# Optimization experiments

Measured on AMD Instinct MI355X. Metric: run time of the kernel, lower is better.

Reference implementation:

```python
import jax, jax.numpy as jnp
import numpy as np

NUM_REL = 3


def _edge_norm(dst, et, n_nodes):
    # PyG RGCNConv default aggr='mean': mean over edges per (dst, relation).
    seg = dst * NUM_REL + et
    cnt = jax.ops.segment_sum(jnp.ones(dst.shape[0], jnp.float32), seg,
                              num_segments=n_nodes * NUM_REL)
    return 1.0 / jnp.maximum(cnt, 1.0)[seg], seg  # [E]


def _rgcn_layer(x, W, root, b, src, dst, et, norm_e, seg, transform_first):
    n = x.shape[0]
    if transform_first:
        # h_r = x @ W_r for all relations, gather message per edge, scatter-add.
        H = jnp.einsum('ni,rio->rno', x, W)          # [R, N, out]
        m = H[et, src] * norm_e[:, None]             # [E, out]
        agg = jax.ops.segment_sum(m, dst, num_segments=n)
    else:
        # mean-aggregate in input space first (mean commutes with linear map).
        m = x[src] * norm_e[:, None]                 # [E, in]
        A = jax.ops.segment_sum(m, seg, num_segments=n * NUM_REL)
        A = A.reshape(n, NUM_REL, -1)                # [N, R, in]
        agg = jnp.einsum('nri,rio->no', A, W)
    return agg + x @ root + b


def _make_params(key, in_c, out_c):
    dims = [(in_c, 1024), (1024, 512), (512, 128)]
    ks = jax.random.split(key, 14)
    p = {}
    for li, (i, o) in enumerate(dims, start=1):
        p[f'W{li}'] = jax.random.normal(ks[3 * li - 3], (NUM_REL, i, o), jnp.float32) * 0.02
        p[f'root{li}'] = jax.random.normal(ks[3 * li - 2], (i, o), jnp.float32) * 0.02
        p[f'b{li}'] = jnp.zeros((o,), jnp.float32)
    p['fc_w'] = jax.random.normal(ks[9], (128, out_c), jnp.float32) * 0.02
    p['fc_b'] = jnp.zeros((out_c,), jnp.float32)
    return p


def setup_inputs() -> dict:
    key = jax.random.key(0)
    N, E, IN_C, OUT_C = 40000, 500000, 256, 21
    k1, k2, k3, k4 = jax.random.split(key, 4)
    inp = {
        'x': jax.random.normal(k1, (N, IN_C), jnp.float32),
        'edge_index': jax.random.randint(k2, (2, E), 0, N, jnp.int64)
            if jax.config.jax_enable_x64 else jax.random.randint(k2, (2, E), 0, N, jnp.int32),
        'edge_type': jax.random.randint(k3, (E,), 0, NUM_REL, jnp.int32),
    }
    inp.update(_make_params(k4, IN_C, OUT_C))
    return inp


def reference(x, edge_index, edge_type, W1, root1, b1, W2, root2, b2,
              W3, root3, b3, fc_w, fc_b):
    src, dst = edge_index[0], edge_index[1]
    et = edge_type
    n = x.shape[0]
    norm_e, seg = _edge_norm(dst, et, n)
    # layer 1: in(256) < out(1024) -> aggregate-first is cheaper
    h = _rgcn_layer(x, W1, root1, b1, src, dst, et, norm_e, seg, transform_first=False)
    h = jax.nn.relu(h)  # dropout is identity in eval mode
    # layer 2: in(1024) > out(512) -> transform-first
    h = _rgcn_layer(h, W2, root2, b2, src, dst, et, norm_e, seg, transform_first=True)
    h = jax.nn.relu(h)
    # layer 3: in(512) > out(128) -> transform-first
    h = _rgcn_layer(h, W3, root3, b3, src, dst, et, norm_e, seg, transform_first=True)
    h = jax.nn.relu(h)
    logits = h @ fc_w + fc_b
    return jax.nn.log_softmax(logits, axis=1)
```

## Files before the change

kernel.cpp:

```cpp
#include <hip/hip_runtime.h>
#include <cstdint>
#include <cstddef>


typedef short bf16x8 __attribute__((ext_vector_type(8)));
typedef float f32x4 __attribute__((ext_vector_type(4)));

#define GF_BIAS 1
#define GF_RELU 2
#define GF_BF16 4

__device__ __forceinline__ unsigned short f2bf(float f) {
    unsigned u = __float_as_uint(f);
    return (unsigned short)((u + 0x7FFFu + ((u >> 16) & 1u)) >> 16);
}
__device__ __forceinline__ float bf2f(unsigned short h) {
    return __uint_as_float((unsigned)h << 16);
}

__global__ __launch_bounds__(256) void zero_kernel(float* __restrict__ p, long n4)
{
    long i = (long)blockIdx.x * 256 + threadIdx.x;
    if (i < n4) ((float4*)p)[i] = make_float4(0.f, 0.f, 0.f, 0.f);
}

__global__ __launch_bounds__(256) void count_kernel(
    const int* __restrict__ dst, const int* __restrict__ et,
    int* __restrict__ cnt, int E)
{
    int e = blockIdx.x * 256 + threadIdx.x;
    if (e < E) atomicAdd(&cnt[dst[e] * 3 + et[e]], 1);
}

__global__ __launch_bounds__(256) void scanA(
    const int* __restrict__ cnt, int* __restrict__ base,
    int* __restrict__ bsum, int S)
{
    __shared__ int sh[256];
    int i = blockIdx.x * 256 + threadIdx.x;
    int v = (i < S) ? cnt[i] : 0;
    sh[threadIdx.x] = v;
    __syncthreads();
#pragma unroll
    for (int off = 1; off < 256; off <<= 1) {
        int t = (threadIdx.x >= off) ? sh[threadIdx.x - off] : 0;
        __syncthreads();
        sh[threadIdx.x] += t;
        __syncthreads();
    }
    if (i < S) base[i] = sh[threadIdx.x] - v;
    if (threadIdx.x == 255) bsum[blockIdx.x] = sh[255];
}

__global__ __launch_bounds__(512) void scanB(int* __restrict__ bsum, int NB)
{
    __shared__ int sh[512];
    int t = threadIdx.x;
    int v = (t < NB) ? bsum[t] : 0;
    sh[t] = v;
    __syncthreads();
#pragma unroll
    for (int off = 1; off < 512; off <<= 1) {
        int u = (t >= off) ? sh[t - off] : 0;
        __syncthreads();
        sh[t] += u;
        __syncthreads();
    }
    if (t < NB) bsum[t] = sh[t] - v;
}

__global__ __launch_bounds__(256) void scanC(
    int* __restrict__ base, const int* __restrict__ bsum, int S)
{
    int i = blockIdx.x * 256 + threadIdx.x;
    if (i < S) base[i] += bsum[blockIdx.x];
}

__global__ __launch_bounds__(256) void fill_kernel(
    const int* __restrict__ src, const int* __restrict__ dst,
    const int* __restrict__ et, const int* __restrict__ base,
    int* __restrict__ ecur, int* __restrict__ elist, int E)
{
    int e = blockIdx.x * 256 + threadIdx.x;
    if (e >= E) return;
    int seg = dst[e] * 3 + et[e];
    int pos = base[seg] + atomicAdd(&ecur[seg], 1);
    elist[pos] = src[e];
}

__global__ __launch_bounds__(256) void transpose_bf16(
    const float* __restrict__ in, unsigned short* __restrict__ out,
    int R, int C, int ldo)
{
    int idx = blockIdx.x * 256 + threadIdx.x;
    if (idx >= R * C) return;
    int j = idx / R, i = idx - j * R;
    out[(size_t)j * ldo + i] = f2bf(in[(size_t)i * C + j]);
}

__global__ __launch_bounds__(256) void conv_bf16(
    const float* __restrict__ s, unsigned short* __restrict__ d, long n8)
{
    long i = (long)blockIdx.x * 256 + threadIdx.x;
    if (i >= n8) return;
    const float* p = s + i * 8;
    float4 a = *(const float4*)p, b = *(const float4*)(p + 4);
    ushort4 o0, o1;
    o0.x = f2bf(a.x); o0.y = f2bf(a.y); o0.z = f2bf(a.z); o0.w = f2bf(a.w);
    o1.x = f2bf(b.x); o1.y = f2bf(b.y); o1.z = f2bf(b.z); o1.w = f2bf(b.w);
    *(ushort4*)(d + i * 8) = o0;
    *(ushort4*)(d + i * 8 + 4) = o1;
}

__global__ __launch_bounds__(256) void make_bias(
    float* __restrict__ dst, const float* __restrict__ src, int nsrc, int ntot)
{
    int i = blockIdx.x * 256 + threadIdx.x;
    if (i < ntot) dst[i] = (i < nsrc) ? src[i] : 0.f;
}

__global__ __launch_bounds__(256) void agg1_kernel(
    const unsigned short* __restrict__ xb, const int* __restrict__ base,
    const int* __restrict__ cnt, const int* __restrict__ elist,
    unsigned short* __restrict__ Xcat)
{
    int n = blockIdx.x;
    int w = threadIdx.x >> 6, l = threadIdx.x & 63;
    if (w == 3) {
        *(ushort4*)&Xcat[(size_t)n * 1024 + 768 + l * 4] =
            *(const ushort4*)&xb[(size_t)n * 256 + l * 4];
        return;
    }
    int seg = n * 3 + w;
    int st = base[seg], len = cnt[seg];
    float norm = 1.0f / (float)(len > 0 ? len : 1);
    float4 s = make_float4(0.f, 0.f, 0.f, 0.f);
    for (int i = 0; i < len; ++i) {
        int sx = elist[st + i];
        ushort4 v = *(const ushort4*)&xb[(size_t)sx * 256 + l * 4];
        s.x += bf2f(v.x); s.y += bf2f(v.y); s.z += bf2f(v.z); s.w += bf2f(v.w);
    }
    ushort4 o;
    o.x = f2bf(s.x * norm); o.y = f2bf(s.y * norm);
    o.z = f2bf(s.z * norm); o.w = f2bf(s.w * norm);
    *(ushort4*)&Xcat[(size_t)n * 1024 + w * 256 + l * 4] = o;
}

__global__ __launch_bounds__(128) void agg2_fused(
    const unsigned short* __restrict__ H2all, unsigned short* __restrict__ h2b,
    const int* __restrict__ base, const int* __restrict__ cnt,
    const int* __restrict__ elist)
{
    int n = blockIdx.x, t = threadIdx.x;
    ushort4 rv = *(const ushort4*)&H2all[(size_t)n * 2048 + t * 4];
    float4 a = make_float4(bf2f(rv.x), bf2f(rv.y), bf2f(rv.z), bf2f(rv.w));
#pragma unroll
    for (int r = 0; r < 3; ++r) {
        int seg = n * 3 + r;
        int st = base[seg], len = cnt[seg];
        float norm = 1.0f / (float)(len > 0 ? len : 1);
        float4 s = make_float4(0.f, 0.f, 0.f, 0.f);
        for (int i = 0; i < len; ++i) {
            int sx = elist[st + i];
            ushort4 v = *(const ushort4*)&H2all[(size_t)sx * 2048 + 512 * (1 + r) + t * 4];
            s.x += bf2f(v.x); s.y += bf2f(v.y); s.z += bf2f(v.z); s.w += bf2f(v.w);
        }
        a.x += s.x * norm; a.y += s.y * norm; a.z += s.z * norm; a.w += s.w * norm;
    }
    ushort4 o;
    o.x = f2bf(fmaxf(a.x, 0.f)); o.y = f2bf(fmaxf(a.y, 0.f));
    o.z = f2bf(fmaxf(a.z, 0.f)); o.w = f2bf(fmaxf(a.w, 0.f));
    *(ushort4*)&h2b[(size_t)n * 512 + t * 4] = o;
}

__global__ __launch_bounds__(128) void agg2_inc(
    const unsigned short* __restrict__ H2q, float* __restrict__ h2acc,
    unsigned short* __restrict__ h2b, const int* __restrict__ base,
    const int* __restrict__ cnt, const int* __restrict__ elist, int r, int last)
{
    int n = blockIdx.x, t = threadIdx.x;
    int seg = n * 3 + r;
    int st = base[seg], len = cnt[seg];
    float norm = 1.0f / (float)(len > 0 ? len : 1);
    float4 s = make_float4(0.f, 0.f, 0.f, 0.f);
    for (int i = 0; i < len; ++i) {
        int sx = elist[st + i];
        ushort4 v = *(const ushort4*)&H2q[(size_t)sx * 512 + t * 4];
        s.x += bf2f(v.x); s.y += bf2f(v.y); s.z += bf2f(v.z); s.w += bf2f(v.w);
    }
    float4 a = *(const float4*)&h2acc[(size_t)n * 512 + t * 4];
    a.x += s.x * norm; a.y += s.y * norm; a.z += s.z * norm; a.w += s.w * norm;
    if (!last) {
        *(float4*)&h2acc[(size_t)n * 512 + t * 4] = a;
    } else {
        ushort4 o;
        o.x = f2bf(fmaxf(a.x, 0.f)); o.y = f2bf(fmaxf(a.y, 0.f));
        o.z = f2bf(fmaxf(a.z, 0.f)); o.w = f2bf(fmaxf(a.w, 0.f));
        *(ushort4*)&h2b[(size_t)n * 512 + t * 4] = o;
    }
}

__global__ __launch_bounds__(64) void agg3_kernel(
    const unsigned short* __restrict__ H3cat, float* __restrict__ h3,
    const int* __restrict__ base, const int* __restrict__ cnt,
    const int* __restrict__ elist)
{
    int n = blockIdx.x;
    int l = threadIdx.x;
    ushort2 rt = *(const ushort2*)&H3cat[(size_t)n * 512 + l * 2];
    float s0 = bf2f(rt.x), s1 = bf2f(rt.y);
#pragma unroll
    for (int r = 0; r < 3; ++r) {
        int seg = n * 3 + r;
        int st = base[seg], len = cnt[seg];
        float norm = 1.0f / (float)(len > 0 ? len : 1);
        float t0 = 0.f, t1 = 0.f;
        for (int i = 0; i < len; ++i) {
            int sx = elist[st + i];
            ushort2 v = *(const ushort2*)&H3cat[(size_t)sx * 512 + 128 * (1 + r) + l * 2];
            t0 += bf2f(v.x); t1 += bf2f(v.y);
        }
        s0 += t0 * norm; s1 += t1 * norm;
    }
    float2 o; o.x = s0; o.y = s1;
    *(float2*)&h3[(size_t)n * 128 + l * 2] = o;
}

__global__ __launch_bounds__(256) void gemm_mfma(
    const unsigned short* __restrict__ A, const unsigned short* __restrict__ Bt,
    const float* __restrict__ bias, void* __restrict__ C,
    int Nout, int K, int ldbt, int flags, int lgGX)
{
    __shared__ short __align__(16) As[8192];
    __shared__ short __align__(16) Bs[8192];
    const int tid = threadIdx.x;
    const int w = tid >> 6, l = tid & 63;

    const int nblk = (int)gridDim.x;
    const int q = nblk >> 3, rem = nblk & 7;
    const int xcd = blockIdx.x & 7, local = blockIdx.x >> 3;
    const int id2 = xcd * q + (xcd < rem ? xcd : rem) + local;
    const int row0 = (id2 >> lgGX) * 128;
    const int col0 = (id2 & ((1 << lgGX) - 1)) * 128;

    const int wm = w >> 1, wn = w & 1;
    const int lr = l >> 3, lc = l & 7;

    f32x4 acc[4][4];
#pragma unroll
    for (int i = 0; i < 4; ++i)
#pragma unroll
        for (int j = 0; j < 4; ++j) acc[i][j] = (f32x4){0.f, 0.f, 0.f, 0.f};

    for (int k0 = 0; k0 < K; k0 += 64) {
        __syncthreads();
#pragma unroll
        for (int i = 0; i < 4; ++i) {
            const int c  = i * 4 + w;
            const int r  = c * 8 + lr;
            const int c8 = lc ^ (r & 7);
            __builtin_amdgcn_global_load_lds(
                (const __attribute__((address_space(1))) void*)
                    (A + (size_t)(row0 + r) * K + k0 + c8 * 8),
                (__attribute__((address_space(3))) void*)(As + c * 512),
                16, 0, 0);
            __builtin_amdgcn_global_load_lds(
                (const __attribute__((address_space(1))) void*)
                    (Bt + (size_t)(col0 + r) * ldbt + k0 + c8 * 8),
                (__attribute__((address_space(3))) void*)(Bs + c * 512),
                16, 0, 0);
        }
        __syncthreads();
#pragma unroll
        for (int ks = 0; ks < 2; ++ks) {
            bf16x8 af[4], bfv[4];
#pragma unroll
            for (int mf = 0; mf < 4; ++mf) {
                int r = wm * 64 + mf * 16 + (l & 15);
                int byt = (r * 128 + ks * 64 + (l >> 4) * 16) ^ ((r & 7) << 4);
                af[mf] = *(const bf16x8*)((const char*)As + byt);
            }
#pragma unroll
            for (int nf = 0; nf < 4; ++nf) {
                int r = wn * 64 + nf * 16 + (l & 15);
                int byt = (r * 128 + ks * 64 + (l >> 4) * 16) ^ ((r & 7) << 4);
                bfv[nf] = *(const bf16x8*)((const char*)Bs + byt);
            }
#pragma unroll
            for (int mf = 0; mf < 4; ++mf)
#pragma unroll
                for (int nf = 0; nf < 4; ++nf)
                    acc[mf][nf] = __builtin_amdgcn_mfma_f32_16x16x32_bf16(
                        af[mf], bfv[nf], acc[mf][nf], 0, 0, 0);
        }
    }

    const int lrow = (l >> 4) * 4;
    const int lcol = l & 15;
#pragma unroll
    for (int mf = 0; mf < 4; ++mf) {
#pragma unroll
        for (int nf = 0; nf < 4; ++nf) {
            int col = col0 + wn * 64 + nf * 16 + lcol;
            float bv = (flags & GF_BIAS) ? bias[col] : 0.f;
#pragma unroll
            for (int rr = 0; rr < 4; ++rr) {
                int row = row0 + wm * 64 + mf * 16 + lrow + rr;
                float v = acc[mf][nf][rr] + bv;
                if (flags & GF_RELU) v = fmaxf(v, 0.f);
                size_t idx = (size_t)row * Nout + col;
                if (flags & GF_BF16) ((unsigned short*)C)[idx] = f2bf(v);
                else                 ((float*)C)[idx] = v;
            }
        }
    }
}

__global__ __launch_bounds__(256) void head_kernel(
    const float* __restrict__ h3, const float* __restrict__ fcw,
    const float* __restrict__ fcb, float* __restrict__ out, int M)
{
    __shared__ float sh[4][128];
    int wid = threadIdx.x >> 6, lane = threadIdx.x & 63;
    int row = blockIdx.x * 4 + wid;
    sh[wid][lane]      = fmaxf(h3[(size_t)row * 128 + lane], 0.f);
    sh[wid][64 + lane] = fmaxf(h3[(size_t)row * 128 + 64 + lane], 0.f);
    __syncthreads();
    float logit = 0.f;
    if (lane < 21) {
        logit = fcb[lane];
#pragma unroll
        for (int k = 0; k < 128; ++k) logit += sh[wid][k] * fcw[k * 21 + lane];
    }
    float v = (lane < 21) ? logit : -INFINITY;
#pragma unroll
    for (int off = 32; off; off >>= 1) v = fmaxf(v, __shfl_xor(v, off));
    float mx = v;
    float ex = (lane < 21) ? expf(logit - mx) : 0.f;
#pragma unroll
    for (int off = 32; off; off >>= 1) ex += __shfl_xor(ex, off);
    if (lane < 21) out[(size_t)row * 21 + lane] = logit - mx - logf(ex);
}

extern "C" void kernel_launch(void* const* d_in, const int* in_sizes, int n_in,
                              void* d_out, int out_size, void* d_ws, size_t ws_size,
                              hipStream_t stream)
{
    const float* x     = (const float*)d_in[0];
    const int*   ei    = (const int*)d_in[1];
    const int*   etp   = (const int*)d_in[2];
    const float* W1    = (const float*)d_in[3];
    const float* root1 = (const float*)d_in[4];
    const float* b1    = (const float*)d_in[5];
    const float* W2    = (const float*)d_in[6];
    const float* root2 = (const float*)d_in[7];
    const float* b2    = (const float*)d_in[8];
    const float* W3    = (const float*)d_in[9];
    const float* root3 = (const float*)d_in[10];
    const float* b3    = (const float*)d_in[11];
    const float* fcw   = (const float*)d_in[12];
    const float* fcb   = (const float*)d_in[13];
    float* out = (float*)d_out;
    (void)n_in; (void)out_size;

    const int N  = in_sizes[0] / 256;
    const int E  = in_sizes[2];
    const int S  = N * 3;
    const int NP = (N + 127) / 128 * 128;
    const int GY = NP / 128;
    const int NB = (S + 255) / 256;
    const int* srcp = ei;
    const int* dstp = ei + E;

    const size_t SZ_X1024 = (size_t)NP * 1024 * 2;
    const size_t SZ_X512b = (size_t)NP * 512 * 2;
    const size_t SZ_X2048 = (size_t)NP * 2048 * 2;
    const size_t SZ_XB    = (size_t)NP * 256 * 2;
    const size_t SZ_H3    = (size_t)NP * 128 * 4;

    char* ws = (char*)d_ws;
    int*            cnt   = (int*)(ws + 0);
    int*            base  = (int*)(ws + 480256);
    int*            elist = (int*)(ws + 960512);
    float*          b2cat = (float*)(ws + 2960512);
    float*          b3cat = (float*)(ws + 2968704);
    unsigned short* W3cat = (unsigned short*)(ws + 2970752);
    unsigned short* W2cat = (unsigned short*)(ws + 3495040);
    const size_t fixed_end = 7689344;
    const size_t FUSED_NEED = 7692288 + SZ_X2048 + SZ_X1024;
    const bool fused = ws_size >= FUSED_NEED;

    char* arena;
    unsigned short *W1t, *xb, *Xcat, *h1b, *H2all, *H2q, *h2b, *H3cat;
    float *h2acc, *h3;
    if (fused) {
        arena = ws + 7692288;
        Xcat  = (unsigned short*)(arena);
        W1t   = (unsigned short*)(arena + SZ_X1024);
        xb    = (unsigned short*)(arena + SZ_X1024 + 2097152);
        h1b   = (unsigned short*)(arena + SZ_X2048);
        H2all = (unsigned short*)(arena);
        h2b   = (unsigned short*)(arena + SZ_X2048);
        H3cat = (unsigned short*)(arena);
        h3    = (float*)(arena + SZ_X512b);
        H2q = nullptr; h2acc = nullptr;
    } else {
        W1t   = (unsigned short*)(ws + fixed_end);
        arena = ws + fixed_end + 2097152 + 2944;
        Xcat  = (unsigned short*)(arena);
        h2acc = (float*)(arena);
        h1b   = (unsigned short*)(arena + SZ_X1024);
        h2b   = (unsigned short*)(arena + SZ_X1024);
        H3cat = (unsigned short*)(arena + SZ_X1024 + SZ_X512b);
        xb    = (unsigned short*)(arena + 2 * SZ_X1024);
        H2q   = (unsigned short*)(arena + 2 * SZ_X1024);
        h3    = (float*)(arena + 2 * SZ_X1024);
        H2all = nullptr;
    }
    int* ecur = (int*)(arena);
    int* bsum = (int*)(arena + 480256);

    zero_kernel<<<(S * 4 / 16 + 255) / 256, 256, 0, stream>>>((float*)cnt, S * 4 / 16);
    zero_kernel<<<(S * 4 / 16 + 255) / 256, 256, 0, stream>>>((float*)ecur, S * 4 / 16);
    count_kernel<<<(E + 255) / 256, 256, 0, stream>>>(dstp, etp, cnt, E);
    scanA<<<NB, 256, 0, stream>>>(cnt, base, bsum, S);
    scanB<<<1, 512, 0, stream>>>(bsum, NB);
    scanC<<<NB, 256, 0, stream>>>(base, bsum, S);
    fill_kernel<<<(E + 255) / 256, 256, 0, stream>>>(srcp, dstp, etp, base, ecur, elist, E);

    transpose_bf16<<<(768 * 1024 + 255) / 256, 256, 0, stream>>>(W1, W1t, 768, 1024, 1024);
    transpose_bf16<<<(256 * 1024 + 255) / 256, 256, 0, stream>>>(root1, W1t + 768, 256, 1024, 1024);
    transpose_bf16<<<(1024 * 512 + 255) / 256, 256, 0, stream>>>(root2, W2cat, 1024, 512, 1024);
    for (int r = 0; r < 3; ++r)
        transpose_bf16<<<(1024 * 512 + 255) / 256, 256, 0, stream>>>(
            W2 + (size_t)r * 524288, W2cat + (size_t)(1 + r) * 524288, 1024, 512, 1024);
    transpose_bf16<<<(512 * 128 + 255) / 256, 256, 0, stream>>>(root3, W3cat, 512, 128, 512);
    for (int r = 0; r < 3; ++r)
        transpose_bf16<<<(512 * 128 + 255) / 256, 256, 0, stream>>>(
            W3 + (size_t)r * 65536, W3cat + (size_t)(1 + r) * 65536, 512, 128, 512);
    make_bias<<<8, 256, 0, stream>>>(b2cat, b2, 512, 2048);
    make_bias<<<2, 256, 0, stream>>>(b3cat, b3, 128, 512);
    conv_bf16<<<(int)(((long)N * 32 + 255) / 256), 256, 0, stream>>>(x, xb, (long)N * 32);

    agg1_kernel<<<N, 256, 0, stream>>>(xb, base, cnt, elist, Xcat);
    gemm_mfma<<<8 * GY, 256, 0, stream>>>(
        Xcat, W1t, b1, h1b, 1024, 1024, 1024, GF_BIAS | GF_RELU | GF_BF16, 3);

    if (fused) {
        gemm_mfma<<<16 * GY, 256, 0, stream>>>(
            h1b, W2cat, b2cat, H2all, 2048, 1024, 1024, GF_BIAS | GF_BF16, 4);
        agg2_fused<<<N, 128, 0, stream>>>(H2all, h2b, base, cnt, elist);
    } else {
        gemm_mfma<<<4 * GY, 256, 0, stream>>>(
            h1b, W2cat, b2, h2acc, 512, 1024, 1024, GF_BIAS, 2);
        for (int r = 0; r < 3; ++r) {
            gemm_mfma<<<4 * GY, 256, 0, stream>>>(
                h1b, W2cat + (size_t)(1 + r) * 524288, nullptr, H2q, 512, 1024, 1024, GF_BF16, 2);
            agg2_inc<<<N, 128, 0, stream>>>(H2q, h2acc, h2b, base, cnt, elist, r, r == 2);
        }
    }

    gemm_mfma<<<4 * GY, 256, 0, stream>>>(
        h2b, W3cat, b3cat, H3cat, 512, 512, 512, GF_BIAS | GF_BF16, 2);
    agg3_kernel<<<N, 64, 0, stream>>>(H3cat, h3, base, cnt, elist);

    head_kernel<<<N / 4, 256, 0, stream>>>(h3, fcw, fcb, out, N);
}
```

Before: 705.4 us.

## Fuse layer-3 aggregation with head, tile weight transposes, drop CSR count buffer

Measured after the change: 675.5 us. 1.04x faster.

```diff
diff --git a/kernel.cpp b/kernel.cpp
--- a/kernel.cpp
+++ b/kernel.cpp
@@ -78,24 +78,83 @@
 
 __global__ __launch_bounds__(256) void fill_kernel(
     const int* __restrict__ src, const int* __restrict__ dst,
-    const int* __restrict__ et, const int* __restrict__ base,
-    int* __restrict__ ecur, int* __restrict__ elist, int E)
+    const int* __restrict__ et, int* __restrict__ base,
+    int* __restrict__ cnt, int* __restrict__ elist, int E, int S)
 {
     int e = blockIdx.x * 256 + threadIdx.x;
+    if (e == 0) base[S] = E;
     if (e >= E) return;
     int seg = dst[e] * 3 + et[e];
-    int pos = base[seg] + atomicAdd(&ecur[seg], 1);
-    elist[pos] = src[e];
-}
-
-__global__ __launch_bounds__(256) void transpose_bf16(
-    const float* __restrict__ in, unsigned short* __restrict__ out,
-    int R, int C, int ldo)
-{
-    int idx = blockIdx.x * 256 + threadIdx.x;
-    if (idx >= R * C) return;
-    int j = idx / R, i = idx - j * R;
-    out[(size_t)j * ldo + i] = f2bf(in[(size_t)i * C + j]);
+    int old = atomicSub(&cnt[seg], 1);
+    elist[base[seg] + old - 1] = src[e];
+}
+
+__global__ __launch_bounds__(256) void tr1_tiled(
+    const float* __restrict__ W1, const float* __restrict__ root1,
+    unsigned short* __restrict__ W1t)
+{
+    __shared__ float sh[32][33];
+    int bk = blockIdx.x & 31, bj = blockIdx.x >> 5;
+    int tc = threadIdx.x & 31, tr = threadIdx.x >> 5;
+    int k0 = bk * 32, j0 = bj * 32;
+#pragma unroll
+    for (int i = 0; i < 4; ++i) {
+        int k = k0 + tr + i * 8;
+        float v = (k < 768) ? W1[(size_t)k * 1024 + j0 + tc]
+                            : root1[(size_t)(k - 768) * 1024 + j0 + tc];
+        sh[tr + i * 8][tc] = v;
+    }
+    __syncthreads();
+#pragma unroll
+    for (int i = 0; i < 4; ++i)
+        W1t[(size_t)(j0 + tr + i * 8) * 1024 + k0 + tc] = f2bf(sh[tc][tr + i * 8]);
+}
+
+__global__ __launch_bounds__(256) void tr2_tiled(
+    const float* __restrict__ root2, const float* __restrict__ W2,
+    unsigned short* __restrict__ W2cat)
+{
+    __shared__ float sh[32][33];
+    int bk = blockIdx.x & 31, br = blockIdx.x >> 5;
+    int tc = threadIdx.x & 31, tr = threadIdx.x >> 5;
+    int k0 = bk * 32, r0 = br * 32;
+    int s = r0 >> 9, j0 = r0 & 511;
+    const float* src = (s == 0) ? root2 : W2 + (size_t)(s - 1) * 524288;
+#pragma unroll
+    for (int i = 0; i < 4; ++i)
+        sh[tr + i * 8][tc] = src[(size_t)(k0 + tr + i * 8) * 512 + j0 + tc];
+    __syncthreads();
+#pragma unroll
+    for (int i = 0; i < 4; ++i)
+        W2cat[(size_t)(r0 + tr + i * 8) * 1024 + k0 + tc] = f2bf(sh[tc][tr + i * 8]);
+}
+
+__global__ __launch_bounds__(256) void tr3_tiled(
+    const float* __restrict__ root3, const float* __restrict__ W3,
+    unsigned short* __restrict__ W3cat)
+{
+    __shared__ float sh[32][33];
+    int bk = blockIdx.x & 15, br = blockIdx.x >> 4;
+    int tc = threadIdx.x & 31, tr = threadIdx.x >> 5;
+    int k0 = bk * 32, r0 = br * 32;
+    int s = r0 >> 7, j0 = r0 & 127;
+    const float* src = (s == 0) ? root3 : W3 + (size_t)(s - 1) * 65536;
+#pragma unroll
+    for (int i = 0; i < 4; ++i)
+        sh[tr + i * 8][tc] = src[(size_t)(k0 + tr + i * 8) * 128 + j0 + tc];
+    __syncthreads();
+#pragma unroll
+    for (int i = 0; i < 4; ++i)
+        W3cat[(size_t)(r0 + tr + i * 8) * 512 + k0 + tc] = f2bf(sh[tc][tr + i * 8]);
+}
+
+__global__ __launch_bounds__(256) void bias_cat(
+    float* __restrict__ b2cat, float* __restrict__ b3cat,
+    const float* __restrict__ b2, const float* __restrict__ b3)
+{
+    int i = blockIdx.x * 256 + threadIdx.x;
+    if (i < 2048) b2cat[i] = (i < 512) ? b2[i] : 0.f;
+    else if (i < 2560) { int j = i - 2048; b3cat[j] = (j < 128) ? b3[j] : 0.f; }
 }
 
 __global__ __launch_bounds__(256) void conv_bf16(
@@ -112,17 +171,9 @@
     *(ushort4*)(d + i * 8 + 4) = o1;
 }
 
-__global__ __launch_bounds__(256) void make_bias(
-    float* __restrict__ dst, const float* __restrict__ src, int nsrc, int ntot)
-{
-    int i = blockIdx.x * 256 + threadIdx.x;
-    if (i < ntot) dst[i] = (i < nsrc) ? src[i] : 0.f;
-}
-
 __global__ __launch_bounds__(256) void agg1_kernel(
     const unsigned short* __restrict__ xb, const int* __restrict__ base,
-    const int* __restrict__ cnt, const int* __restrict__ elist,
-    unsigned short* __restrict__ Xcat)
+    const int* __restrict__ elist, unsigned short* __restrict__ Xcat)
 {
     int n = blockIdx.x;
     int w = threadIdx.x >> 6, l = threadIdx.x & 63;
@@ -132,7 +183,7 @@
         return;
     }
     int seg = n * 3 + w;
-    int st = base[seg], len = cnt[seg];
+    int st = base[seg], len = base[seg + 1] - st;
     float norm = 1.0f / (float)(len > 0 ? len : 1);
     float4 s = make_float4(0.f, 0.f, 0.f, 0.f);
     for (int i = 0; i < len; ++i) {
@@ -148,8 +199,7 @@
 
 __global__ __launch_bounds__(128) void agg2_fused(
     const unsigned short* __restrict__ H2all, unsigned short* __restrict__ h2b,
-    const int* __restrict__ base, const int* __restrict__ cnt,
-    const int* __restrict__ elist)
+    const int* __restrict__ base, const int* __restrict__ elist)
 {
     int n = blockIdx.x, t = threadIdx.x;
     ushort4 rv = *(const ushort4*)&H2all[(size_t)n * 2048 + t * 4];
@@ -157,7 +207,7 @@
 #pragma unroll
     for (int r = 0; r < 3; ++r) {
         int seg = n * 3 + r;
-        int st = base[seg], len = cnt[seg];
+        int st = base[seg], len = base[seg + 1] - st;
         float norm = 1.0f / (float)(len > 0 ? len : 1);
         float4 s = make_float4(0.f, 0.f, 0.f, 0.f);
         for (int i = 0; i < len; ++i) {
@@ -176,11 +226,11 @@
 __global__ __launch_bounds__(128) void agg2_inc(
     const unsigned short* __restrict__ H2q, float* __restrict__ h2acc,
     unsigned short* __restrict__ h2b, const int* __restrict__ base,
-    const int* __restrict__ cnt, const int* __restrict__ elist, int r, int last)
+    const int* __restrict__ elist, int r, int last)
 {
     int n = blockIdx.x, t = threadIdx.x;
     int seg = n * 3 + r;
-    int st = base[seg], len = cnt[seg];
+    int st = base[seg], len = base[seg + 1] - st;
     float norm = 1.0f / (float)(len > 0 ? len : 1);
     float4 s = make_float4(0.f, 0.f, 0.f, 0.f);
     for (int i = 0; i < len; ++i) {
@@ -200,36 +250,52 @@
     }
 }
 
-__global__ __launch_bounds__(64) void agg3_kernel(
-    const unsigned short* __restrict__ H3cat, float* __restrict__ h3,
-    const int* __restrict__ base, const int* __restrict__ cnt,
-    const int* __restrict__ elist)
-{
-    int n = blockIdx.x;
-    int l = threadIdx.x;
-    ushort2 rt = *(const ushort2*)&H3cat[(size_t)n * 512 + l * 2];
+__global__ __launch_bounds__(256) void agg3_head(
+    const unsigned short* __restrict__ H3cat, const float* __restrict__ fcw,
+    const float* __restrict__ fcb, const int* __restrict__ base,
+    const int* __restrict__ elist, float* __restrict__ out)
+{
+    __shared__ float sh[4][128];
+    int wid = threadIdx.x >> 6, lane = threadIdx.x & 63;
+    int n = blockIdx.x * 4 + wid;
+    ushort2 rt = *(const ushort2*)&H3cat[(size_t)n * 512 + lane * 2];
     float s0 = bf2f(rt.x), s1 = bf2f(rt.y);
 #pragma unroll
     for (int r = 0; r < 3; ++r) {
         int seg = n * 3 + r;
-        int st = base[seg], len = cnt[seg];
+        int st = base[seg], len = base[seg + 1] - st;
         float norm = 1.0f / (float)(len > 0 ? len : 1);
         float t0 = 0.f, t1 = 0.f;
         for (int i = 0; i < len; ++i) {
             int sx = elist[st + i];
-            ushort2 v = *(const ushort2*)&H3cat[(size_t)sx * 512 + 128 * (1 + r) + l * 2];
+            ushort2 v = *(const ushort2*)&H3cat[(size_t)sx * 512 + 128 * (1 + r) + lane * 2];
             t0 += bf2f(v.x); t1 += bf2f(v.y);
         }
         s0 += t0 * norm; s1 += t1 * norm;
     }
-    float2 o; o.x = s0; o.y = s1;
-    *(float2*)&h3[(size_t)n * 128 + l * 2] = o;
+    sh[wid][lane * 2]     = fmaxf(s0, 0.f);
+    sh[wid][lane * 2 + 1] = fmaxf(s1, 0.f);
+    __syncthreads();
+    float logit = 0.f;
+    if (lane < 21) {
+        logit = fcb[lane];
+#pragma unroll
+        for (int k = 0; k < 128; ++k) logit += sh[wid][k] * fcw[k * 21 + lane];
+    }
+    float v = (lane < 21) ? logit : -INFINITY;
+#pragma unroll
+    for (int off = 32; off; off >>= 1) v = fmaxf(v, __shfl_xor(v, off));
+    float mx = v;
+    float ex = (lane < 21) ? expf(logit - mx) : 0.f;
+#pragma unroll
+    for (int off = 32; off; off >>= 1) ex += __shfl_xor(ex, off);
+    if (lane < 21) out[(size_t)n * 21 + lane] = logit - mx - logf(ex);
 }
 
 __global__ __launch_bounds__(256) void gemm_mfma(
     const unsigned short* __restrict__ A, const unsigned short* __restrict__ Bt,
     const float* __restrict__ bias, void* __restrict__ C,
-    int Nout, int K, int ldbt, int flags, int lgGX)
+    int Nout, int K, int flags, int lgGX)
 {
     __shared__ short __align__(16) As[8192];
     __shared__ short __align__(16) Bs[8192];
@@ -266,7 +332,7 @@
                 16, 0, 0);
             __builtin_amdgcn_global_load_lds(
                 (const __attribute__((address_space(1))) void*)
-                    (Bt + (size_t)(col0 + r) * ldbt + k0 + c8 * 8),
+                    (Bt + (size_t)(col0 + r) * K + k0 + c8 * 8),
                 (__attribute__((address_space(3))) void*)(Bs + c * 512),
                 16, 0, 0);
         }
@@ -314,32 +380,6 @@
             }
         }
     }
-}
-
-__global__ __launch_bounds__(256) void head_kernel(
-    const float* __restrict__ h3, const float* __restrict__ fcw,
-    const float* __restrict__ fcb, float* __restrict__ out, int M)
-{
-    __shared__ float sh[4][128];
-    int wid = threadIdx.x >> 6, lane = threadIdx.x & 63;
-    int row = blockIdx.x * 4 + wid;
-    sh[wid][lane]      = fmaxf(h3[(size_t)row * 128 + lane], 0.f);
-    sh[wid][64 + lane] = fmaxf(h3[(size_t)row * 128 + 64 + lane], 0.f);
-    __syncthreads();
-    float logit = 0.f;
-    if (lane < 21) {
-        logit = fcb[lane];
-#pragma unroll
-        for (int k = 0; k < 128; ++k) logit += sh[wid][k] * fcw[k * 21 + lane];
-    }
-    float v = (lane < 21) ? logit : -INFINITY;
-#pragma unroll
-    for (int off = 32; off; off >>= 1) v = fmaxf(v, __shfl_xor(v, off));
-    float mx = v;
-    float ex = (lane < 21) ? expf(logit - mx) : 0.f;
-#pragma unroll
-    for (int off = 32; off; off >>= 1) ex += __shfl_xor(ex, off);
-    if (lane < 21) out[(size_t)row * 21 + lane] = logit - mx - logf(ex);
 }
 
 extern "C" void kernel_launch(void* const* d_in, const int* in_sizes, int n_in,
@@ -363,20 +403,18 @@
     float* out = (float*)d_out;
     (void)n_in; (void)out_size;
 
-    const int N  = in_sizes[0] / 256;
-    const int E  = in_sizes[2];
-    const int S  = N * 3;
-    const int NP = (N + 127) / 128 * 128;
-    const int GY = NP / 128;
-    const int NB = (S + 255) / 256;
+    const int N   = in_sizes[0] / 256;
+    const int E   = in_sizes[2];
+    const int S   = N * 3;
+    const int NP  = (N + 127) / 128 * 128;
+    const int GY  = NP / 128;
+    const int NB  = (S + 255) / 256;
     const int* srcp = ei;
     const int* dstp = ei + E;
 
     const size_t SZ_X1024 = (size_t)NP * 1024 * 2;
     const size_t SZ_X512b = (size_t)NP * 512 * 2;
     const size_t SZ_X2048 = (size_t)NP * 2048 * 2;
-    const size_t SZ_XB    = (size_t)NP * 256 * 2;
-    const size_t SZ_H3    = (size_t)NP * 128 * 4;
 
     char* ws = (char*)d_ws;
     int*            cnt   = (int*)(ws + 0);
@@ -392,7 +430,7 @@
 
     char* arena;
     unsigned short *W1t, *xb, *Xcat, *h1b, *H2all, *H2q, *h2b, *H3cat;
-    float *h2acc, *h3;
+    float* h2acc;
     if (fused) {
         arena = ws + 7692288;
         Xcat  = (unsigned short*)(arena);
@@ -402,11 +440,10 @@
         H2all = (unsigned short*)(arena);
         h2b   = (unsigned short*)(arena + SZ_X2048);
         H3cat = (unsigned short*)(arena);
-        h3    = (float*)(arena + SZ_X512b);
         H2q = nullptr; h2acc = nullptr;
     } else {
         W1t   = (unsigned short*)(ws + fixed_end);
-        arena = ws + fixed_end + 2097152 + 2944;
+        arena = ws + 9789440;
         Xcat  = (unsigned short*)(arena);
         h2acc = (float*)(arena);
         h1b   = (unsigned short*)(arena + SZ_X1024);
@@ -414,55 +451,42 @@
         H3cat = (unsigned short*)(arena + SZ_X1024 + SZ_X512b);
         xb    = (unsigned short*)(arena + 2 * SZ_X1024);
         H2q   = (unsigned short*)(arena + 2 * SZ_X1024);
-        h3    = (float*)(arena + 2 * SZ_X1024);
         H2all = nullptr;
     }
-    int* ecur = (int*)(arena);
-    int* bsum = (int*)(arena + 480256);
-
-    zero_kernel<<<(S * 4 / 16 + 255) / 256, 256, 0, stream>>>((float*)cnt, S * 4 / 16);
-    zero_kernel<<<(S * 4 / 16 + 255) / 256, 256, 0, stream>>>((float*)ecur, S * 4 / 16);
+    int* bsum = (int*)(arena);
+
+    zero_kernel<<<(30016 + 255) / 256, 256, 0, stream>>>((float*)cnt, 30016);
     count_kernel<<<(E + 255) / 256, 256, 0, stream>>>(dstp, etp, cnt, E);
     scanA<<<NB, 256, 0, stream>>>(cnt, base, bsum, S);
     scanB<<<1, 512, 0, stream>>>(bsum, NB);
     scanC<<<NB, 256, 0, stream>>>(base, bsum, S);
-    fill_kernel<<<(E + 255) / 256, 256, 0, stream>>>(srcp, dstp, etp, base, ecur, elist, E);
-
-    transpose_bf16<<<(768 * 1024 + 255) / 256, 256, 0, stream>>>(W1, W1t, 768, 1024, 1024);
-    transpose_bf16<<<(256 * 1024 + 255) / 256, 256, 0, stream>>>(root1, W1t + 768, 256, 1024, 1024);
-    transpose_bf16<<<(1024 * 512 + 255) / 256, 256, 0, stream>>>(root2, W2cat, 1024, 512, 1024);
-    for (int r = 0; r < 3; ++r)
-        transpose_bf16<<<(1024 * 512 + 255) / 256, 256, 0, stream>>>(
-            W2 + (size_t)r * 524288, W2cat + (size_t)(1 + r) * 524288, 1024, 512, 1024);
-    transpose_bf16<<<(512 * 128 + 255) / 256, 256, 0, stream>>>(root3, W3cat, 512, 128, 512);
-    for (int r = 0; r < 3; ++r)
-        transpose_bf16<<<(512 * 128 + 255) / 256, 256, 0, stream>>>(
-            W3 + (size_t)r * 65536, W3cat + (size_t)(1 + r) * 65536, 512, 128, 512);
-    make_bias<<<8, 256, 0, stream>>>(b2cat, b2, 512, 2048);
-    make_bias<<<2, 256, 0, stream>>>(b3cat, b3, 128, 512);
+    fill_kernel<<<(E + 255) / 256, 256, 0, stream>>>(srcp, dstp, etp, base, cnt, elist, E, S);
+
+    tr1_tiled<<<1024, 256, 0, stream>>>(W1, root1, W1t);
+    tr2_tiled<<<2048, 256, 0, stream>>>(root2, W2, W2cat);
+    tr3_tiled<<<256, 256, 0, stream>>>(root3, W3, W3cat);
+    bias_cat<<<10, 256, 0, stream>>>(b2cat, b3cat, b2, b3);
     conv_bf16<<<(int)(((long)N * 32 + 255) / 256), 256, 0, stream>>>(x, xb, (long)N * 32);
 
-    agg1_kernel<<<N, 256, 0, stream>>>(xb, base, cnt, elist, Xcat);
+    agg1_kernel<<<N, 256, 0, stream>>>(xb, base, elist, Xcat);
     gemm_mfma<<<8 * GY, 256, 0, stream>>>(
-        Xcat, W1t, b1, h1b, 1024, 1024, 1024, GF_BIAS | GF_RELU | GF_BF16, 3);
+        Xcat, W1t, b1, h1b, 1024, 1024, GF_BIAS | GF_RELU | GF_BF16, 3);
 
     if (fused) {
         gemm_mfma<<<16 * GY, 256, 0, stream>>>(
-            h1b, W2cat, b2cat, H2all, 2048, 1024, 1024, GF_BIAS | GF_BF16, 4);
-        agg2_fused<<<N, 128, 0, stream>>>(H2all, h2b, base, cnt, elist);
+            h1b, W2cat, b2cat, H2all, 2048, 1024, GF_BIAS | GF_BF16, 4);
+        agg2_fused<<<N, 128, 0, stream>>>(H2all, h2b, base, elist);
     } else {
         gemm_mfma<<<4 * GY, 256, 0, stream>>>(
-            h1b, W2cat, b2, h2acc, 512, 1024, 1024, GF_BIAS, 2);
+            h1b, W2cat, b2, h2acc, 512, 1024, GF_BIAS, 2);
         for (int r = 0; r < 3; ++r) {
             gemm_mfma<<<4 * GY, 256, 0, stream>>>(
-                h1b, W2cat + (size_t)(1 + r) * 524288, nullptr, H2q, 512, 1024, 1024, GF_BF16, 2);
-            agg2_inc<<<N, 128, 0, stream>>>(H2q, h2acc, h2b, base, cnt, elist, r, r == 2);
+                h1b, W2cat + (size_t)(1 + r) * 524288, nullptr, H2q, 512, 1024, GF_BF16, 2);
+            agg2_inc<<<N, 128, 0, stream>>>(H2q, h2acc, h2b, base, elist, r, r == 2);
         }
     }
 
     gemm_mfma<<<4 * GY, 256, 0, stream>>>(
-        h2b, W3cat, b3cat, H3cat, 512, 512, 512, GF_BIAS | GF_BF16, 2);
-    agg3_kernel<<<N, 64, 0, stream>>>(H3cat, h3, base, cnt, elist);
-
-    head_kernel<<<N / 4, 256, 0, stream>>>(h3, fcw, fcb, out, N);
-}
+        h2b, W3cat, b3cat, H3cat, 512, 512, GF_BIAS | GF_BF16, 2);
+    agg3_head<<<N / 4, 256, 0, stream>>>(H3cat, fcw, fcb, base, elist, out);
+}
```
